# Kernel tuning notes

Hardware: AMD Instinct MI355X
Metric: run time of the kernel (lower is better)

## Reference

```python
import jax, jax.numpy as jnp
import numpy as np

D_MODEL = 1024
NUM_HEADS = 16
THETA = 10000.0
BATCH = 2
SEQ = 2048


def setup_inputs() -> dict:
    key = jax.random.key(0)
    ks = jax.random.split(key, 5)
    std = (2.0 / (D_MODEL + D_MODEL)) ** 0.5
    mk = lambda k: jax.random.truncated_normal(k, -3.0, 3.0, (D_MODEL, D_MODEL), jnp.float32) * std
    return {
        'x': jax.random.normal(ks[0], (BATCH, SEQ, D_MODEL), jnp.float32),
        'Wq': mk(ks[1]),
        'Wk': mk(ks[2]),
        'Wv': mk(ks[3]),
        'Wo': mk(ks[4]),
        'token_positions': jnp.arange(SEQ, dtype=jnp.int32),
    }


def _apply_rope(x, token_positions, theta):
    # x: (B, H, S, d_k)
    d_k = x.shape[-1]
    freq = 1.0 / theta ** (jnp.arange(0, d_k, 2, dtype=jnp.float32) / d_k)  # (d_k//2,)
    freqs = token_positions.astype(jnp.float32)[:, None] * freq[None, :]   # (S, d_k//2)
    cos, sin = jnp.cos(freqs), jnp.sin(freqs)
    x_real = x[..., 0::2]
    x_imag = x[..., 1::2]
    rot_real = x_real * cos - x_imag * sin
    rot_imag = x_real * sin + x_imag * cos
    # interleave back: (..., d_k//2, 2) -> (..., d_k)
    out = jnp.stack([rot_real, rot_imag], axis=-1)
    return out.reshape(x.shape)


def reference(x, Wq, Wk, Wv, Wo, token_positions):
    B, S, D = x.shape
    H = NUM_HEADS
    d_k = D // H

    def split_heads(t):
        return t.reshape(B, S, H, d_k).transpose(0, 2, 1, 3)  # (B, H, S, d_k)

    Q = split_heads(jnp.einsum('bsd,od->bso', x, Wq))
    K = split_heads(jnp.einsum('bsd,od->bso', x, Wk))
    V = split_heads(jnp.einsum('bsd,od->bso', x, Wv))

    Q = _apply_rope(Q, token_positions, THETA)
    K = _apply_rope(K, token_positions, THETA)

    # naive materialized attention with causal mask, faithful to source
    scores = jnp.einsum('bhqd,bhkd->bhqk', Q, K)
    causal = jnp.tril(jnp.ones((S, S), dtype=bool))  # True = attend
    scores = jnp.where(causal[None, None], scores, -jnp.inf)
    scores = scores / jnp.sqrt(jnp.asarray(d_k, scores.dtype))
    probs = jax.nn.softmax(scores, axis=-1)
    attn = jnp.einsum('bhqk,bhkd->bhqd', probs, V)  # (B, H, S, d_v)

    attn = attn.transpose(0, 2, 1, 3).reshape(B, S, D)
    return jnp.einsum('bsd,od->bso', attn, Wo)
```

## Files before the change

### kernel.cpp

```cpp
#include <hip/hip_runtime.h>
#include <hip/hip_bf16.h>
#include <math.h>

#define NUM_HEADS 16
#define DK 64
#define SEQ 2048
#define BATCHN 2
#define DM 1024
#define BS (BATCHN*SEQ)
#define LSCALE 0.18033688011112042f

typedef __bf16 bf16x8 __attribute__((ext_vector_type(8)));
typedef float floatx4 __attribute__((ext_vector_type(4)));
typedef unsigned short ushort;
typedef unsigned int uint;

__device__ __forceinline__ ushort f2bu(float f){
    union { __hip_bfloat16 h; ushort u; } cv; cv.h = __float2bfloat16(f); return cv.u;
}
__device__ __forceinline__ uint packbf(float a, float b){
    return (uint)f2bu(a) | ((uint)f2bu(b) << 16);
}
__device__ __forceinline__ float bu2f(ushort u){
    union { uint u; float f; } cv; cv.u = (uint)u << 16; return cv.f;
}
__device__ __forceinline__ uint cvtpk(float lo, float hi){
    uint r; asm("v_cvt_pk_bf16_f32 %0, %1, %2" : "=v"(r) : "v"(lo), "v"(hi));
    return r;
}
__device__ __forceinline__ void gl16(const void* g, void* l){
    __builtin_amdgcn_global_load_lds(
        (const __attribute__((address_space(1))) unsigned int*)g,
        (__attribute__((address_space(3))) unsigned int*)l, 16, 0, 0);
}

__global__ __launch_bounds__(256)
void castall(const float* __restrict__ x,  const float* __restrict__ wq,
             const float* __restrict__ wk, const float* __restrict__ wv,
             const float* __restrict__ wo, const int* __restrict__ pos,
             ushort* __restrict__ xb, ushort* __restrict__ wqkb,
             ushort* __restrict__ wvb, ushort* __restrict__ wob,
             float2* __restrict__ tab)
{
    int bid = blockIdx.x;
    if (bid >= 4096) {
        int idx = (bid - 4096)*256 + threadIdx.x;
        int s = idx >> 5, i = idx & 31;
        float invf = expf(-0.28782313662425575f * (float)i);
        float ang = (float)pos[s] * invf;
        float sn, cs; sincosf(ang, &sn, &cs);
        tab[idx] = make_float2(cs, sn);
        return;
    }
    const float* src; ushort* dst; int off;
    if (bid < 2048)      { src = x;  dst = xb;             off = bid; }
    else if (bid < 2560) { src = wq; dst = wqkb;           off = bid - 2048; }
    else if (bid < 3072) { src = wk; dst = wqkb + 1048576; off = bid - 2560; }
    else if (bid < 3584) { src = wv; dst = wvb;            off = bid - 3072; }
    else                 { src = wo; dst = wob;            off = bid - 3584; }
    int i = off*2048 + threadIdx.x*8;
    float4 a = *(const float4*)(src+i);
    float4 b = *(const float4*)(src+i+4);
    uint4 o;
    o.x = packbf(a.x, a.y);
    o.y = packbf(a.z, a.w);
    o.z = packbf(b.x, b.y);
    o.w = packbf(b.z, b.w);
    *(uint4*)(dst+i) = o;
}

__global__ __launch_bounds__(256)
void proj_fused(const ushort* __restrict__ xb, const ushort* __restrict__ Wqkb,
                const ushort* __restrict__ Wvb, ushort* __restrict__ Qb,
                ushort* __restrict__ VTp, const float2* __restrict__ rope)
{
    __shared__ ushort As[128][32];
    __shared__ ushort Bs[128][32];

    const int bid = blockIdx.x;
    const ushort* A; const ushort* W; int row0, col0, mode;
    if (bid < 512) { A = xb;  W = Wqkb; row0 = (bid >> 4) * 128;
                     col0 = (bid & 15) * 128;  mode = 1; }
    else           { int i = bid - 512; A = Wvb; W = xb;
                     row0 = (i >> 5) * 128; col0 = (i & 31) * 128; mode = 2; }

    const int t = threadIdx.x;
    const int w = t >> 6;
    const int L = t & 63;
    const int lr = L & 15;
    const int lq = L >> 4;
    const int wrow = w * 32;

    floatx4 acc[2][8];
    #pragma unroll
    for (int i = 0; i < 2; ++i)
        #pragma unroll
        for (int j = 0; j < 8; ++j)
            acc[i][j] = (floatx4){0.f,0.f,0.f,0.f};

    const int rr = t >> 2, ko = (t & 3) * 8;
    const ushort* ga = A + (size_t)(row0 + rr) * DM + ko;
    const ushort* gb = W + (size_t)(col0 + rr) * DM + ko;

    for (int k0 = 0; k0 < DM; k0 += 32) {
        __syncthreads();
        gl16(ga + k0,                    &As[rr][ko]);
        gl16(ga + k0 + (size_t)64*DM,    &As[rr + 64][ko]);
        gl16(gb + k0,                    &Bs[rr][ko]);
        gl16(gb + k0 + (size_t)64*DM,    &Bs[rr + 64][ko]);
        __syncthreads();

        bf16x8 aF0 = *(const bf16x8*)&As[wrow + lr][lq*8];
        bf16x8 aF1 = *(const bf16x8*)&As[wrow + 16 + lr][lq*8];
        #pragma unroll
        for (int tc = 0; tc < 8; ++tc) {
            bf16x8 bF = *(const bf16x8*)&Bs[tc*16 + lr][lq*8];
            acc[0][tc] = __builtin_amdgcn_mfma_f32_16x16x32_bf16(aF0, bF, acc[0][tc], 0, 0, 0);
            acc[1][tc] = __builtin_amdgcn_mfma_f32_16x16x32_bf16(aF1, bF, acc[1][tc], 0, 0, 0);
        }
    }

    if (mode == 2) {
        #pragma unroll
        for (int tr = 0; tr < 2; ++tr)
            #pragma unroll
            for (int tc = 0; tc < 8; ++tc)
                #pragma unroll
                for (int r = 0; r < 4; ++r) {
                    int m = row0 + wrow + tr*16 + lq*4 + r;
                    int c = col0 + tc*16 + lr;
                    VTp[(size_t)m * BS + c] = f2bu(acc[tr][tc][r]);
                }
    } else {
        const int mat = col0 >> 10;
        const int base_hh = (col0 & 1023) >> 6;
        ushort* out = Qb + (size_t)mat * (BATCHN*NUM_HEADS*SEQ*DK);
        const float qscale = mat ? 1.f : LSCALE;
        #pragma unroll
        for (int tr = 0; tr < 2; ++tr)
            #pragma unroll
            for (int tc = 0; tc < 8; ++tc)
                #pragma unroll
                for (int r = 0; r < 4; ++r) {
                    int m = row0 + wrow + tr*16 + lq*4 + r;
                    int b = m >> 11;
                    int s = m & (SEQ - 1);
                    int dd = (tc*16 + lr) & 63;
                    int hh = base_hh + (tc >> 2);
                    float v = acc[tr][tc][r];
                    float o = __shfl_xor(v, 1, 64);
                    float2 cs = rope[s*32 + (dd >> 1)];
                    float rv = (dd & 1) ? fmaf(o, cs.y,  v * cs.x)
                                        : fmaf(-o, cs.y, v * cs.x);
                    out[((size_t)((b*NUM_HEADS + hh)*SEQ + s))*DK + dd] =
                        f2bu(rv * qscale);
                }
    }
}

__global__ __launch_bounds__(256)
void gemm_out(const ushort* __restrict__ A, const ushort* __restrict__ W,
              float* __restrict__ out)
{
    __shared__ ushort As[128][32];
    __shared__ ushort Bs[64][32];

    const int t = threadIdx.x;
    const int w = t >> 6;
    const int L = t & 63;
    const int lr = L & 15;
    const int lq = L >> 4;
    const int row0 = blockIdx.y * 128;
    const int col0 = blockIdx.x * 64;
    const int wrow = w * 32;

    floatx4 acc[2][4];
    #pragma unroll
    for (int i = 0; i < 2; ++i)
        #pragma unroll
        for (int j = 0; j < 4; ++j)
            acc[i][j] = (floatx4){0.f,0.f,0.f,0.f};

    const int rr = t >> 2, ko = (t & 3) * 8;
    const ushort* ga = A + (size_t)(row0 + rr) * DM + ko;
    const ushort* gb = W + (size_t)(col0 + rr) * DM + ko;

    for (int k0 = 0; k0 < DM; k0 += 32) {
        __syncthreads();
        gl16(ga + k0,                 &As[rr][ko]);
        gl16(ga + k0 + (size_t)64*DM, &As[rr + 64][ko]);
        gl16(gb + k0,                 &Bs[rr][ko]);
        __syncthreads();

        bf16x8 aF0 = *(const bf16x8*)&As[wrow + lr][lq*8];
        bf16x8 aF1 = *(const bf16x8*)&As[wrow + 16 + lr][lq*8];
        #pragma unroll
        for (int tc = 0; tc < 4; ++tc) {
            bf16x8 bF = *(const bf16x8*)&Bs[tc*16 + lr][lq*8];
            acc[0][tc] = __builtin_amdgcn_mfma_f32_16x16x32_bf16(aF0, bF, acc[0][tc], 0, 0, 0);
            acc[1][tc] = __builtin_amdgcn_mfma_f32_16x16x32_bf16(aF1, bF, acc[1][tc], 0, 0, 0);
        }
    }

    #pragma unroll
    for (int tr = 0; tr < 2; ++tr)
        #pragma unroll
        for (int tc = 0; tc < 4; ++tc)
            #pragma unroll
            for (int r = 0; r < 4; ++r) {
                int m = row0 + wrow + tr*16 + lq*4 + r;
                int c = col0 + tc*16 + lr;
                out[(size_t)m * DM + c] = acc[tr][tc][r];
            }
}

__global__ __launch_bounds__(128)
void attn_mfma(const ushort* __restrict__ Qb, const ushort* __restrict__ Kb,
               const ushort* __restrict__ VT, ushort* __restrict__ attnb,
               ushort* __restrict__ Opart, float* __restrict__ lpart)
{
    __shared__ ushort Ks[64*64];
    __shared__ ushort Vs[64*64];

    const int t = threadIdx.x;
    const int w = t >> 6;
    const int L = t & 63;
    const int lr = L & 15, lq = L >> 4;
    const int h  = blockIdx.y;
    const int b  = blockIdx.z;

    int qt, chunk, nch;
    {
        const int bx = blockIdx.x;
        if (bx < 8)       { qt = bx;              chunk = 0;     nch = 1; }
        else if (bx < 24) { int i = bx - 8;  qt = 8  + (i>>1); chunk = i&1;        nch = 2; }
        else if (bx < 48) { int i = bx - 24; int q3 = i/3; qt = 16 + q3; chunk = i - q3*3; nch = 3; }
        else              { int i = bx - 48; qt = 24 + (i>>2); chunk = i&3;        nch = 4; }
    }
    const int nt = qt + 1;
    const int t0 = (nt * chunk) / nch;
    const int t1 = (nt * (chunk + 1)) / nch;
    const int q0 = qt * 64;
    const int qw = q0 + w * 32;
    const size_t qkbase = (size_t)(b*NUM_HEADS + h) * SEQ * DK;

    bf16x8 qA0, qA1, qB0, qB1;
    {
        const ushort* qp = Qb + qkbase + (size_t)(qw + lr) * DK + lq*8;
        qA0 = *(const bf16x8*)qp;
        qA1 = *(const bf16x8*)(qp + 32);
        qB0 = *(const bf16x8*)(qp + 16*DK);
        qB1 = *(const bf16x8*)(qp + 16*DK + 32);
    }

    bf16x8 ones8;
    {
        union { uint u[4]; bf16x8 v; } o;
        o.u[0] = o.u[1] = o.u[2] = o.u[3] = 0x3f803f80u;
        ones8 = o.v;
    }

    floatx4 O0[4], O1[4];
    #pragma unroll
    for (int g = 0; g < 4; ++g) {
        O0[g] = (floatx4){0.f,0.f,0.f,0.f};
        O1[g] = (floatx4){0.f,0.f,0.f,0.f};
    }
    floatx4 lA = (floatx4){0.f,0.f,0.f,0.f};
    floatx4 lB = (floatx4){0.f,0.f,0.f,0.f};

    const int sr = t >> 3, t7 = t & 7;
    const int kwb  = (sr*64 + t7*8) ^ ((sr & 7) << 3);
    const int pc0  = ((t7 >> 2) << 3) | ((t7 & 1) << 2) | ((t7 >> 1) & 1);
    const int vwb0 = (sr*64 + pc0*4)     ^ ((sr & 7) << 3);
    const int vwb1 = (sr*64 + pc0*4 + 8) ^ ((sr & 7) << 3);
    const ushort* kpt = Kb + qkbase + (size_t)sr * DK + t7*8;
    const ushort* vpt = VT + ((size_t)(h*DK + sr)) * BS + b*SEQ + t7*8;

    const int kro0 = (lr*64 + lq*8)      ^ ((lr & 7) << 3);
    const int kro1 = (lr*64 + 32 + lq*8) ^ ((lr & 7) << 3);

    uint4 kv0, kv1, kv2, kv3, vv0, vv1, vv2, vv3;

#define GLOAD(T)                                                              \
    {                                                                         \
        const ushort* kg = kpt + (size_t)(T) * 64 * DK;                       \
        const ushort* vg = vpt + (T) * 64;                                    \
        kv0 = *(const uint4*)(kg);                                            \
        kv1 = *(const uint4*)(kg + 16*DK);                                    \
        kv2 = *(const uint4*)(kg + 32*DK);                                    \
        kv3 = *(const uint4*)(kg + 48*DK);                                    \
        vv0 = *(const uint4*)(vg);                                            \
        vv1 = *(const uint4*)(vg + (size_t)16*BS);                            \
        vv2 = *(const uint4*)(vg + (size_t)32*BS);                            \
        vv3 = *(const uint4*)(vg + (size_t)48*BS);                            \
    }

#define STAGE()                                                               \
    {                                                                         \
        *(uint4*)&Ks[kwb]        = kv0;                                       \
        *(uint4*)&Ks[kwb + 1024] = kv1;                                       \
        *(uint4*)&Ks[kwb + 2048] = kv2;                                       \
        *(uint4*)&Ks[kwb + 3072] = kv3;                                       \
        *(uint2*)&Vs[vwb0]        = make_uint2(vv0.x, vv0.y);                 \
        *(uint2*)&Vs[vwb1]        = make_uint2(vv0.z, vv0.w);                 \
        *(uint2*)&Vs[vwb0 + 1024] = make_uint2(vv1.x, vv1.y);                 \
        *(uint2*)&Vs[vwb1 + 1024] = make_uint2(vv1.z, vv1.w);                 \
        *(uint2*)&Vs[vwb0 + 2048] = make_uint2(vv2.x, vv2.y);                 \
        *(uint2*)&Vs[vwb1 + 2048] = make_uint2(vv2.z, vv2.w);                 \
        *(uint2*)&Vs[vwb0 + 3072] = make_uint2(vv3.x, vv3.y);                 \
        *(uint2*)&Vs[vwb1 + 3072] = make_uint2(vv3.z, vv3.w);                 \
    }

#define COMPUTE(LASTT)                                                        \
    {                                                                         \
        uint2 pk0[4], pk1[4];                                                 \
        _Pragma("unroll")                                                     \
        for (int g = 0; g < 4; ++g) {                                         \
            bf16x8 kf0 = *(const bf16x8*)&Ks[kro0 + g*1024];                  \
            bf16x8 kf1 = *(const bf16x8*)&Ks[kro1 + g*1024];                  \
            floatx4 s0 = (floatx4){0.f,0.f,0.f,0.f};                          \
            s0 = __builtin_amdgcn_mfma_f32_16x16x32_bf16(kf0, qA0, s0,0,0,0); \
            s0 = __builtin_amdgcn_mfma_f32_16x16x32_bf16(kf1, qA1, s0,0,0,0); \
            floatx4 s1 = (floatx4){0.f,0.f,0.f,0.f};                          \
            s1 = __builtin_amdgcn_mfma_f32_16x16x32_bf16(kf0, qB0, s1,0,0,0); \
            s1 = __builtin_amdgcn_mfma_f32_16x16x32_bf16(kf1, qB1, s1,0,0,0); \
            float a0 = __builtin_amdgcn_exp2f(s0[0]);                         \
            float a1 = __builtin_amdgcn_exp2f(s0[1]);                         \
            float a2 = __builtin_amdgcn_exp2f(s0[2]);                         \
            float a3 = __builtin_amdgcn_exp2f(s0[3]);                         \
            float b0 = __builtin_amdgcn_exp2f(s1[0]);                         \
            float b1 = __builtin_amdgcn_exp2f(s1[1]);                         \
            float b2 = __builtin_amdgcn_exp2f(s1[2]);                         \
            float b3 = __builtin_amdgcn_exp2f(s1[3]);                         \
            if (LASTT) {                                                      \
                const int kbase = g*16 + lq*4;                                \
                a0 = (kbase + 0 <= lim0) ? a0 : 0.f;                          \
                a1 = (kbase + 1 <= lim0) ? a1 : 0.f;                          \
                a2 = (kbase + 2 <= lim0) ? a2 : 0.f;                          \
                a3 = (kbase + 3 <= lim0) ? a3 : 0.f;                          \
                b0 = (kbase + 0 <= lim1) ? b0 : 0.f;                          \
                b1 = (kbase + 1 <= lim1) ? b1 : 0.f;                          \
                b2 = (kbase + 2 <= lim1) ? b2 : 0.f;                          \
                b3 = (kbase + 3 <= lim1) ? b3 : 0.f;                          \
            }                                                                 \
            pk0[g] = make_uint2(cvtpk(a0, a1), cvtpk(a2, a3));                \
            pk1[g] = make_uint2(cvtpk(b0, b1), cvtpk(b2, b3));                \
        }                                                                     \
        _Pragma("unroll")                                                     \
        for (int c = 0; c < 2; ++c) {                                         \
            union { uint u[4]; bf16x8 v; } a0u, a1u;                          \
            a0u.u[0] = pk0[2*c].x;   a0u.u[1] = pk0[2*c].y;                   \
            a0u.u[2] = pk0[2*c+1].x; a0u.u[3] = pk0[2*c+1].y;                 \
            a1u.u[0] = pk1[2*c].x;   a1u.u[1] = pk1[2*c].y;                   \
            a1u.u[2] = pk1[2*c+1].x; a1u.u[3] = pk1[2*c+1].y;                 \
            lA = __builtin_amdgcn_mfma_f32_16x16x32_bf16(a0u.v, ones8, lA,0,0,0); \
            lB = __builtin_amdgcn_mfma_f32_16x16x32_bf16(a1u.v, ones8, lB,0,0,0); \
            const int vro = c ? kro1 : kro0;                                  \
            _Pragma("unroll")                                                 \
            for (int g2 = 0; g2 < 4; ++g2) {                                  \
                bf16x8 vf = *(const bf16x8*)&Vs[vro + g2*1024];               \
                O0[g2] = __builtin_amdgcn_mfma_f32_16x16x32_bf16(a0u.v, vf, O0[g2],0,0,0); \
                O1[g2] = __builtin_amdgcn_mfma_f32_16x16x32_bf16(a1u.v, vf, O1[g2],0,0,0); \
            }                                                                 \
        }                                                                     \
    }

    GLOAD(t0);
    const bool haslast = (t1 == nt);
    const int tmain = haslast ? t1 - 1 : t1;
    {
        const int lim0 = 0, lim1 = 0;
        for (int tile = t0; tile < tmain; ++tile) {
            __syncthreads();
            STAGE();
            __syncthreads();
            if (tile + 1 < t1) GLOAD(tile + 1);
            COMPUTE(false);
        }
    }
    if (haslast) {
        __syncthreads();
        STAGE();
        __syncthreads();
        const int lim0 = qw + lr - (nt - 1)*64;
        const int lim1 = lim0 + 16;
        COMPUTE(true);
    }
#undef GLOAD
#undef STAGE
#undef COMPUTE

    if (nch == 1) {
        #pragma unroll
        for (int r = 0; r < 4; ++r) {
            float li0 = 1.f / lA[r];
            float li1 = 1.f / lB[r];
            int s0r = qw + lq*4 + r;
            int s1r = qw + 16 + lq*4 + r;
            #pragma unroll
            for (int g2 = 0; g2 < 4; ++g2) {
                attnb[((size_t)(b*SEQ + s0r))*DM + h*DK + g2*16 + lr] = f2bu(O0[g2][r] * li0);
                attnb[((size_t)(b*SEQ + s1r))*DM + h*DK + g2*16 + lr] = f2bu(O1[g2][r] * li1);
            }
        }
    } else {
        const int slot = ((b*NUM_HEADS + h)*24 + (qt - 8))*4 + chunk;
        ushort* Op = Opart + (size_t)slot * 4096;
        #pragma unroll
        for (int r = 0; r < 4; ++r) {
            int ql0 = w*32 + lq*4 + r;
            int ql1 = w*32 + 16 + lq*4 + r;
            #pragma unroll
            for (int g2 = 0; g2 < 4; ++g2) {
                Op[ql0*64 + g2*16 + lr] = f2bu(O0[g2][r]);
                Op[ql1*64 + g2*16 + lr] = f2bu(O1[g2][r]);
            }
        }
        if (lr == 0) {
            #pragma unroll
            for (int r = 0; r < 4; ++r) {
                lpart[(size_t)slot*64 + w*32 + lq*4 + r]      = lA[r];
                lpart[(size_t)slot*64 + w*32 + 16 + lq*4 + r] = lB[r];
            }
        }
    }
}

__global__ __launch_bounds__(256)
void combine(const ushort* __restrict__ Opart, const float* __restrict__ lpart,
             ushort* __restrict__ attnb)
{
    int gx = blockIdx.x;
    int qti = gx % 24, bh = gx / 24;
    int h = bh & 15, b = bh >> 4;
    int qt = 8 + qti;
    int nch = (qt >> 3) + 1;
    int tid = threadIdx.x;
    int row = tid >> 2, c0 = (tid & 3) * 16;
    const int base_slot = (bh*24 + qti)*4;

    float acc[16];
    #pragma unroll
    for (int e = 0; e < 16; ++e) acc[e] = 0.f;
    float l = 0.f;

    for (int c = 0; c < nch; ++c) {
        const ushort* Op = Opart + (size_t)(base_slot + c)*4096 + row*64 + c0;
        uint4 u0 = *(const uint4*)(Op);
        uint4 u1 = *(const uint4*)(Op + 8);
        const ushort* h0 = (const ushort*)&u0;
        const ushort* h1 = (const ushort*)&u1;
        #pragma unroll
        for (int e = 0; e < 8; ++e) { acc[e]   += bu2f(h0[e]); }
        #pragma unroll
        for (int e = 0; e < 8; ++e) { acc[8+e] += bu2f(h1[e]); }
        l += lpart[(size_t)(base_slot + c)*64 + row];
    }
    float li = 1.f / l;
    int s = qt*64 + row;
    ushort* dst = attnb + ((size_t)(b*SEQ + s))*DM + h*DK + c0;
    #pragma unroll
    for (int e = 0; e < 16; ++e) dst[e] = f2bu(acc[e] * li);
}

extern "C" void kernel_launch(void* const* d_in, const int* in_sizes, int n_in,
                              void* d_out, int out_size, void* d_ws, size_t ws_size,
                              hipStream_t stream) {
    const float* x   = (const float*)d_in[0];
    const float* Wq  = (const float*)d_in[1];
    const float* Wk  = (const float*)d_in[2];
    const float* Wv  = (const float*)d_in[3];
    const float* Wo  = (const float*)d_in[4];
    const int*   pos = (const int*)d_in[5];
    float* out = (float*)d_out;

    const size_t MB = 1u << 20;
    char* ws = (char*)d_ws;
    ushort* xb    = (ushort*)(ws);
    ushort* Wqkb  = (ushort*)(ws +  8*MB);
    ushort* Wvb   = (ushort*)(ws + 12*MB);
    ushort* Opart = (ushort*)(ws);
    float*  lpart = (float*)(ws + 24*MB);
    ushort* Qb    = (ushort*)(ws + 25*MB);
    ushort* Kb    = (ushort*)(ws + 33*MB);
    ushort* VT    = (ushort*)(ws + 41*MB);
    ushort* attnb = (ushort*)(ws + 49*MB);
    float2* ropeT = (float2*)(ws + 57*MB);
    ushort* Wob   = (ushort*)(ws + 58*MB);

    dim3 blk(256);
    castall<<<4352, blk, 0, stream>>>(x, Wq, Wk, Wv, Wo, pos,
                                      xb, Wqkb, Wvb, Wob, ropeT);

    proj_fused<<<768, blk, 0, stream>>>(xb, Wqkb, Wvb, Qb, VT, ropeT);

    attn_mfma<<<dim3(80, NUM_HEADS, BATCHN), dim3(128), 0, stream>>>(Qb, Kb, VT, attnb,
                                                                     Opart, lpart);
    combine<<<768, blk, 0, stream>>>(Opart, lpart, attnb);

    gemm_out<<<dim3(16,32), blk, 0, stream>>>(attnb, Wob, out);
}
```

Measured before the change: 189.8 us.

## Double-buffer LDS tiles with XOR swizzle in projection and output GEMMs

Both the fused QKV projection GEMM and the output projection GEMM now use two LDS buffers. The next k-tile's global-to-LDS loads are issued before computing on the current tile, so memory latency overlaps with MFMA work and one barrier per iteration is removed. The LDS layout is also XOR-swizzled on the 8-element column chunk to reduce bank conflicts on fragment reads. In exchange, LDS use per block doubles, which may lower occupancy, and explicit waitcnt and barrier handling is added.

```diff
diff --git a/kernel.cpp b/kernel.cpp
--- a/kernel.cpp
+++ b/kernel.cpp
@@ -74,8 +74,8 @@
                 const ushort* __restrict__ Wvb, ushort* __restrict__ Qb,
                 ushort* __restrict__ VTp, const float2* __restrict__ rope)
 {
-    __shared__ ushort As[128][32];
-    __shared__ ushort Bs[128][32];
+    __shared__ ushort As[2*128*32];
+    __shared__ ushort Bs[2*128*32];
 
     const int bid = blockIdx.x;
     const ushort* A; const ushort* W; int row0, col0, mode;
@@ -98,27 +98,47 @@
         for (int j = 0; j < 8; ++j)
             acc[i][j] = (floatx4){0.f,0.f,0.f,0.f};
 
-    const int rr = t >> 2, ko = (t & 3) * 8;
+    const int rr = t >> 2, cb = t & 3;
+    const int ko = (cb ^ ((rr >> 1) & 3)) * 8;
+    const int ldst = rr*32 + cb*8;
     const ushort* ga = A + (size_t)(row0 + rr) * DM + ko;
     const ushort* gb = W + (size_t)(col0 + rr) * DM + ko;
 
+    const int co = (lq*8) ^ (((lr >> 1) & 3) << 3);
+
+#define STG(BUF, K0)                                                          \
+    {                                                                         \
+        gl16(ga + (K0),                 &As[(BUF)*4096 + ldst]);              \
+        gl16(ga + (K0) + (size_t)64*DM, &As[(BUF)*4096 + 2048 + ldst]);       \
+        gl16(gb + (K0),                 &Bs[(BUF)*4096 + ldst]);              \
+        gl16(gb + (K0) + (size_t)64*DM, &Bs[(BUF)*4096 + 2048 + ldst]);       \
+    }
+
+    STG(0, 0)
+    asm volatile("s_waitcnt vmcnt(0)" ::: "memory");
+    __builtin_amdgcn_sched_barrier(0);
+    __builtin_amdgcn_s_barrier();
+
+    int cur = 0;
     for (int k0 = 0; k0 < DM; k0 += 32) {
-        __syncthreads();
-        gl16(ga + k0,                    &As[rr][ko]);
-        gl16(ga + k0 + (size_t)64*DM,    &As[rr + 64][ko]);
-        gl16(gb + k0,                    &Bs[rr][ko]);
-        gl16(gb + k0 + (size_t)64*DM,    &Bs[rr + 64][ko]);
-        __syncthreads();
-
-        bf16x8 aF0 = *(const bf16x8*)&As[wrow + lr][lq*8];
-        bf16x8 aF1 = *(const bf16x8*)&As[wrow + 16 + lr][lq*8];
+        const int nxt = cur ^ 1;
+        if (k0 + 32 < DM) STG(nxt, k0 + 32)
+        const ushort* Ac = As + cur*4096;
+        const ushort* Bc = Bs + cur*4096;
+        bf16x8 aF0 = *(const bf16x8*)&Ac[(wrow + lr)*32 + co];
+        bf16x8 aF1 = *(const bf16x8*)&Ac[(wrow + 16 + lr)*32 + co];
         #pragma unroll
         for (int tc = 0; tc < 8; ++tc) {
-            bf16x8 bF = *(const bf16x8*)&Bs[tc*16 + lr][lq*8];
+            bf16x8 bF = *(const bf16x8*)&Bc[(tc*16 + lr)*32 + co];
             acc[0][tc] = __builtin_amdgcn_mfma_f32_16x16x32_bf16(aF0, bF, acc[0][tc], 0, 0, 0);
             acc[1][tc] = __builtin_amdgcn_mfma_f32_16x16x32_bf16(aF1, bF, acc[1][tc], 0, 0, 0);
         }
-    }
+        asm volatile("s_waitcnt vmcnt(0) lgkmcnt(0)" ::: "memory");
+        __builtin_amdgcn_sched_barrier(0);
+        __builtin_amdgcn_s_barrier();
+        cur = nxt;
+    }
+#undef STG
 
     if (mode == 2) {
         #pragma unroll
@@ -162,8 +182,8 @@
 void gemm_out(const ushort* __restrict__ A, const ushort* __restrict__ W,
               float* __restrict__ out)
 {
-    __shared__ ushort As[128][32];
-    __shared__ ushort Bs[64][32];
+    __shared__ ushort As[2*128*32];
+    __shared__ ushort Bs[2*64*32];
 
     const int t = threadIdx.x;
     const int w = t >> 6;
@@ -181,26 +201,46 @@
         for (int j = 0; j < 4; ++j)
             acc[i][j] = (floatx4){0.f,0.f,0.f,0.f};
 
-    const int rr = t >> 2, ko = (t & 3) * 8;
+    const int rr = t >> 2, cb = t & 3;
+    const int ko = (cb ^ ((rr >> 1) & 3)) * 8;
+    const int ldst = rr*32 + cb*8;
     const ushort* ga = A + (size_t)(row0 + rr) * DM + ko;
     const ushort* gb = W + (size_t)(col0 + rr) * DM + ko;
 
+    const int co = (lq*8) ^ (((lr >> 1) & 3) << 3);
+
+#define STG(BUF, K0)                                                          \
+    {                                                                         \
+        gl16(ga + (K0),                 &As[(BUF)*4096 + ldst]);              \
+        gl16(ga + (K0) + (size_t)64*DM, &As[(BUF)*4096 + 2048 + ldst]);       \
+        gl16(gb + (K0),                 &Bs[(BUF)*2048 + ldst]);              \
+    }
+
+    STG(0, 0)
+    asm volatile("s_waitcnt vmcnt(0)" ::: "memory");
+    __builtin_amdgcn_sched_barrier(0);
+    __builtin_amdgcn_s_barrier();
+
+    int cur = 0;
     for (int k0 = 0; k0 < DM; k0 += 32) {
-        __syncthreads();
-        gl16(ga + k0,                 &As[rr][ko]);
-        gl16(ga + k0 + (size_t)64*DM, &As[rr + 64][ko]);
-        gl16(gb + k0,                 &Bs[rr][ko]);
-        __syncthreads();
-
-        bf16x8 aF0 = *(const bf16x8*)&As[wrow + lr][lq*8];
-        bf16x8 aF1 = *(const bf16x8*)&As[wrow + 16 + lr][lq*8];
+        const int nxt = cur ^ 1;
+        if (k0 + 32 < DM) STG(nxt, k0 + 32)
+        const ushort* Ac = As + cur*4096;
+        const ushort* Bc = Bs + cur*2048;
+        bf16x8 aF0 = *(const bf16x8*)&Ac[(wrow + lr)*32 + co];
+        bf16x8 aF1 = *(const bf16x8*)&Ac[(wrow + 16 + lr)*32 + co];
         #pragma unroll
         for (int tc = 0; tc < 4; ++tc) {
-            bf16x8 bF = *(const bf16x8*)&Bs[tc*16 + lr][lq*8];
+            bf16x8 bF = *(const bf16x8*)&Bc[(tc*16 + lr)*32 + co];
             acc[0][tc] = __builtin_amdgcn_mfma_f32_16x16x32_bf16(aF0, bF, acc[0][tc], 0, 0, 0);
             acc[1][tc] = __builtin_amdgcn_mfma_f32_16x16x32_bf16(aF1, bF, acc[1][tc], 0, 0, 0);
         }
-    }
+        asm volatile("s_waitcnt vmcnt(0) lgkmcnt(0)" ::: "memory");
+        __builtin_amdgcn_sched_barrier(0);
+        __builtin_amdgcn_s_barrier();
+        cur = nxt;
+    }
+#undef STG
 
     #pragma unroll
     for (int tr = 0; tr < 2; ++tr)
```

After: 194.4 us. 1.02x slower.

## Shrink GEMM tiles to 64x64, swizzle LDS, and remap block order

Applied to the files above, without the earlier changes.

Both projection and output GEMMs move from 128x128 / 128x64 tiles to 64x64 tiles. Each wave now owns one 16-row strip with four MFMA accumulators, and grid sizes grow to 3072 and 1024 blocks. LDS rows get an XOR swizzle on the 8-element column chunks to reduce bank conflicts on fragment reads. Block IDs are permuted with (bx&7)*N + bx>>3, which looks aimed at spreading neighbouring tiles across XCDs. Smaller tiles raise occupancy and parallelism, but they halve data reuse per LDS load and so increase global/L2 traffic.

```diff
diff --git a/kernel.cpp b/kernel.cpp
--- a/kernel.cpp
+++ b/kernel.cpp
@@ -74,87 +74,81 @@
                 const ushort* __restrict__ Wvb, ushort* __restrict__ Qb,
                 ushort* __restrict__ VTp, const float2* __restrict__ rope)
 {
-    __shared__ ushort As[128][32];
-    __shared__ ushort Bs[128][32];
-
-    const int bid = blockIdx.x;
+    __shared__ ushort As[64*32];
+    __shared__ ushort Bs[64*32];
+
+    const int bx = blockIdx.x;
+    const int bid = (bx & 7) * 384 + (bx >> 3);
+
     const ushort* A; const ushort* W; int row0, col0, mode;
-    if (bid < 512) { A = xb;  W = Wqkb; row0 = (bid >> 4) * 128;
-                     col0 = (bid & 15) * 128;  mode = 1; }
-    else           { int i = bid - 512; A = Wvb; W = xb;
-                     row0 = (i >> 5) * 128; col0 = (i & 31) * 128; mode = 2; }
+    if (bid < 2048) { A = xb;  W = Wqkb; row0 = (bid >> 5) * 64;
+                      col0 = (bid & 31) * 64;  mode = 1; }
+    else            { int i = bid - 2048; A = Wvb; W = xb;
+                      row0 = (i >> 6) * 64; col0 = (i & 63) * 64; mode = 2; }
 
     const int t = threadIdx.x;
     const int w = t >> 6;
     const int L = t & 63;
     const int lr = L & 15;
     const int lq = L >> 4;
-    const int wrow = w * 32;
-
-    floatx4 acc[2][8];
-    #pragma unroll
-    for (int i = 0; i < 2; ++i)
-        #pragma unroll
-        for (int j = 0; j < 8; ++j)
-            acc[i][j] = (floatx4){0.f,0.f,0.f,0.f};
-
-    const int rr = t >> 2, ko = (t & 3) * 8;
+
+    floatx4 acc[4];
+    #pragma unroll
+    for (int j = 0; j < 4; ++j) acc[j] = (floatx4){0.f,0.f,0.f,0.f};
+
+    const int rr = t >> 2, cb = t & 3;
+    const int ko = (cb ^ ((rr >> 1) & 3)) * 8;
+    const int ldst = rr*32 + cb*8;
     const ushort* ga = A + (size_t)(row0 + rr) * DM + ko;
     const ushort* gb = W + (size_t)(col0 + rr) * DM + ko;
 
+    const int co = (lq*8) ^ (((lr >> 1) & 3) << 3);
+    const int arow = (w*16 + lr)*32;
+
     for (int k0 = 0; k0 < DM; k0 += 32) {
         __syncthreads();
-        gl16(ga + k0,                    &As[rr][ko]);
-        gl16(ga + k0 + (size_t)64*DM,    &As[rr + 64][ko]);
-        gl16(gb + k0,                    &Bs[rr][ko]);
-        gl16(gb + k0 + (size_t)64*DM,    &Bs[rr + 64][ko]);
-        __syncthreads();
-
-        bf16x8 aF0 = *(const bf16x8*)&As[wrow + lr][lq*8];
-        bf16x8 aF1 = *(const bf16x8*)&As[wrow + 16 + lr][lq*8];
-        #pragma unroll
-        for (int tc = 0; tc < 8; ++tc) {
-            bf16x8 bF = *(const bf16x8*)&Bs[tc*16 + lr][lq*8];
-            acc[0][tc] = __builtin_amdgcn_mfma_f32_16x16x32_bf16(aF0, bF, acc[0][tc], 0, 0, 0);
-            acc[1][tc] = __builtin_amdgcn_mfma_f32_16x16x32_bf16(aF1, bF, acc[1][tc], 0, 0, 0);
+        gl16(ga + k0, &As[ldst]);
+        gl16(gb + k0, &Bs[ldst]);
+        __syncthreads();
+
+        bf16x8 aF = *(const bf16x8*)&As[arow + co];
+        #pragma unroll
+        for (int tc = 0; tc < 4; ++tc) {
+            bf16x8 bF = *(const bf16x8*)&Bs[(tc*16 + lr)*32 + co];
+            acc[tc] = __builtin_amdgcn_mfma_f32_16x16x32_bf16(aF, bF, acc[tc], 0, 0, 0);
         }
     }
 
     if (mode == 2) {
         #pragma unroll
-        for (int tr = 0; tr < 2; ++tr)
+        for (int tc = 0; tc < 4; ++tc)
             #pragma unroll
-            for (int tc = 0; tc < 8; ++tc)
-                #pragma unroll
-                for (int r = 0; r < 4; ++r) {
-                    int m = row0 + wrow + tr*16 + lq*4 + r;
-                    int c = col0 + tc*16 + lr;
-                    VTp[(size_t)m * BS + c] = f2bu(acc[tr][tc][r]);
-                }
+            for (int r = 0; r < 4; ++r) {
+                int m = row0 + w*16 + lq*4 + r;
+                int c = col0 + tc*16 + lr;
+                VTp[(size_t)m * BS + c] = f2bu(acc[tc][r]);
+            }
     } else {
         const int mat = col0 >> 10;
-        const int base_hh = (col0 & 1023) >> 6;
+        const int hh  = (col0 & 1023) >> 6;
         ushort* out = Qb + (size_t)mat * (BATCHN*NUM_HEADS*SEQ*DK);
         const float qscale = mat ? 1.f : LSCALE;
         #pragma unroll
-        for (int tr = 0; tr < 2; ++tr)
+        for (int tc = 0; tc < 4; ++tc)
             #pragma unroll
-            for (int tc = 0; tc < 8; ++tc)
-                #pragma unroll
-                for (int r = 0; r < 4; ++r) {
-                    int m = row0 + wrow + tr*16 + lq*4 + r;
-                    int b = m >> 11;
-                    int s = m & (SEQ - 1);
-                    int dd = (tc*16 + lr) & 63;
-                    int hh = base_hh + (tc >> 2);
-                    float v = acc[tr][tc][r];
-                    float o = __shfl_xor(v, 1, 64);
-                    float2 cs = rope[s*32 + (dd >> 1)];
-                    float rv = (dd & 1) ? fmaf(o, cs.y,  v * cs.x)
-                                        : fmaf(-o, cs.y, v * cs.x);
-                    out[((size_t)((b*NUM_HEADS + hh)*SEQ + s))*DK + dd] =
-                        f2bu(rv * qscale);
-                }
+            for (int r = 0; r < 4; ++r) {
+                int m = row0 + w*16 + lq*4 + r;
+                int b = m >> 11;
+                int s = m & (SEQ - 1);
+                int dd = tc*16 + lr;
+                float v = acc[tc][r];
+                float o = __shfl_xor(v, 1, 64);
+                float2 cs = rope[s*32 + (dd >> 1)];
+                float rv = (dd & 1) ? fmaf(o, cs.y,  v * cs.x)
+                                    : fmaf(-o, cs.y, v * cs.x);
+                out[((size_t)((b*NUM_HEADS + hh)*SEQ + s))*DK + dd] =
+                    f2bu(rv * qscale);
+            }
     }
 }
 
@@ -162,56 +156,55 @@
 void gemm_out(const ushort* __restrict__ A, const ushort* __restrict__ W,
               float* __restrict__ out)
 {
-    __shared__ ushort As[128][32];
-    __shared__ ushort Bs[64][32];
+    __shared__ ushort As[64*32];
+    __shared__ ushort Bs[64*32];
+
+    const int bx = blockIdx.x;
+    const int bid = (bx & 7) * 128 + (bx >> 3);
+    const int row0 = (bid >> 4) * 64;
+    const int col0 = (bid & 15) * 64;
 
     const int t = threadIdx.x;
     const int w = t >> 6;
     const int L = t & 63;
     const int lr = L & 15;
     const int lq = L >> 4;
-    const int row0 = blockIdx.y * 128;
-    const int col0 = blockIdx.x * 64;
-    const int wrow = w * 32;
-
-    floatx4 acc[2][4];
-    #pragma unroll
-    for (int i = 0; i < 2; ++i)
-        #pragma unroll
-        for (int j = 0; j < 4; ++j)
-            acc[i][j] = (floatx4){0.f,0.f,0.f,0.f};
-
-    const int rr = t >> 2, ko = (t & 3) * 8;
+
+    floatx4 acc[4];
+    #pragma unroll
+    for (int j = 0; j < 4; ++j) acc[j] = (floatx4){0.f,0.f,0.f,0.f};
+
+    const int rr = t >> 2, cb = t & 3;
+    const int ko = (cb ^ ((rr >> 1) & 3)) * 8;
+    const int ldst = rr*32 + cb*8;
     const ushort* ga = A + (size_t)(row0 + rr) * DM + ko;
     const ushort* gb = W + (size_t)(col0 + rr) * DM + ko;
 
+    const int co = (lq*8) ^ (((lr >> 1) & 3) << 3);
+    const int arow = (w*16 + lr)*32;
+
     for (int k0 = 0; k0 < DM; k0 += 32) {
         __syncthreads();
-        gl16(ga + k0,                 &As[rr][ko]);
-        gl16(ga + k0 + (size_t)64*DM, &As[rr + 64][ko]);
-        gl16(gb + k0,                 &Bs[rr][ko]);
-        __syncthreads();
-
-        bf16x8 aF0 = *(const bf16x8*)&As[wrow + lr][lq*8];
-        bf16x8 aF1 = *(const bf16x8*)&As[wrow + 16 + lr][lq*8];
+        gl16(ga + k0, &As[ldst]);
+        gl16(gb + k0, &Bs[ldst]);
+        __syncthreads();
+
+        bf16x8 aF = *(const bf16x8*)&As[arow + co];
         #pragma unroll
         for (int tc = 0; tc < 4; ++tc) {
-            bf16x8 bF = *(const bf16x8*)&Bs[tc*16 + lr][lq*8];
-            acc[0][tc] = __builtin_amdgcn_mfma_f32_16x16x32_bf16(aF0, bF, acc[0][tc], 0, 0, 0);
-            acc[1][tc] = __builtin_amdgcn_mfma_f32_16x16x32_bf16(aF1, bF, acc[1][tc], 0, 0, 0);
-        }
-    }
-
-    #pragma unroll
-    for (int tr = 0; tr < 2; ++tr)
-        #pragma unroll
-        for (int tc = 0; tc < 4; ++tc)
-            #pragma unroll
-            for (int r = 0; r < 4; ++r) {
-                int m = row0 + wrow + tr*16 + lq*4 + r;
-                int c = col0 + tc*16 + lr;
-                out[(size_t)m * DM + c] = acc[tr][tc][r];
-            }
+            bf16x8 bF = *(const bf16x8*)&Bs[(tc*16 + lr)*32 + co];
+            acc[tc] = __builtin_amdgcn_mfma_f32_16x16x32_bf16(aF, bF, acc[tc], 0, 0, 0);
+        }
+    }
+
+    #pragma unroll
+    for (int tc = 0; tc < 4; ++tc)
+        #pragma unroll
+        for (int r = 0; r < 4; ++r) {
+            int m = row0 + w*16 + lq*4 + r;
+            int c = col0 + tc*16 + lr;
+            out[(size_t)m * DM + c] = acc[tc][r];
+        }
 }
 
 __global__ __launch_bounds__(128)
@@ -493,11 +486,11 @@
     castall<<<4352, blk, 0, stream>>>(x, Wq, Wk, Wv, Wo, pos,
                                       xb, Wqkb, Wvb, Wob, ropeT);
 
-    proj_fused<<<768, blk, 0, stream>>>(xb, Wqkb, Wvb, Qb, VT, ropeT);
+    proj_fused<<<3072, blk, 0, stream>>>(xb, Wqkb, Wvb, Qb, VT, ropeT);
 
     attn_mfma<<<dim3(80, NUM_HEADS, BATCHN), dim3(128), 0, stream>>>(Qb, Kb, VT, attnb,
                                                                      Opart, lpart);
     combine<<<768, blk, 0, stream>>>(Opart, lpart, attnb);
 
-    gemm_out<<<dim3(16,32), blk, 0, stream>>>(attnb, Wob, out);
-}
+    gemm_out<<<1024, blk, 0, stream>>>(attnb, Wob, out);
+}
```

Measured after the change: 200.9 us. 1.06x slower.
